# Optimization experiments

Measured on AMD Instinct MI355X. Metric: run time of the kernel, lower is better.

The kernel has to match this reference:

```python
import jax, jax.numpy as jnp
import numpy as np

WIDTH = 768
HEAD = 64

def setup_inputs() -> dict:
    key = jax.random.key(0)
    ks = jax.random.split(key, 8)
    x = jax.random.normal(ks[0], (8, 2048, WIDTH), dtype=jnp.float32)
    mask = jax.random.randint(ks[1], (2048, 2048), 0, 2, dtype=jnp.int32)
    s = 1.0 / np.sqrt(WIDTH)
    Wq = jax.random.normal(ks[2], (WIDTH, HEAD), dtype=jnp.float32) * s
    Wk = jax.random.normal(ks[3], (WIDTH, HEAD), dtype=jnp.float32) * s
    Wv = jax.random.normal(ks[4], (WIDTH, HEAD), dtype=jnp.float32) * s
    bq = jax.random.normal(ks[5], (HEAD,), dtype=jnp.float32) * 0.01
    bk = jax.random.normal(ks[6], (HEAD,), dtype=jnp.float32) * 0.01
    bv = jax.random.normal(ks[7], (HEAD,), dtype=jnp.float32) * 0.01
    return {"x": x, "Wq": Wq, "bq": bq, "Wk": Wk, "bk": bk, "Wv": Wv, "bv": bv, "mask": mask}

def reference(x, Wq, bq, Wk, bk, Wv, bv, mask) -> jnp.ndarray:
    # x: [B, N, width]; projections -> [B, N, head]
    Q = jnp.einsum('bnw,wh->bnh', x, Wq) + bq
    K = jnp.einsum('bnw,wh->bnh', x, Wk) + bk
    V = jnp.einsum('bnw,wh->bnh', x, Wv) + bv
    scale = 1.0 / jnp.sqrt(jnp.asarray(Q.shape[-1], dtype=Q.dtype))
    scores = jnp.einsum('bqh,bkh->bqk', Q, K) * scale  # [B, N, N]
    scores = jnp.where(mask == 0, -jnp.inf, scores)
    attn = jax.nn.softmax(scores, axis=-1)
    return jnp.einsum('bqk,bkh->bqh', attn, V)
```

## Files before the change

kernel.cpp:

```cpp
#include <hip/hip_runtime.h>

typedef short  s8v   __attribute__((ext_vector_type(8)));
typedef float  f32x4 __attribute__((ext_vector_type(4)));

#define SEQ 2048
#define WID 768

__device__ __forceinline__ unsigned fbits(float f) {
    union { float f; unsigned u; } v; v.f = f; return v.u;
}
__device__ __forceinline__ float bitsf(unsigned u) {
    union { unsigned u; float f; } v; v.u = u; return v.f;
}
__device__ __forceinline__ unsigned short f2b(float f) {
    unsigned u = fbits(f);
    return (unsigned short)((u + 0x7FFFu + ((u >> 16) & 1u)) >> 16);
}
__device__ __forceinline__ unsigned packRNE(float a, float b) {
    unsigned ta = fbits(a) + 0x7FFFu + ((fbits(a) >> 16) & 1u);
    unsigned tb = fbits(b) + 0x7FFFu + ((fbits(b) >> 16) & 1u);
    return __builtin_amdgcn_perm(tb, ta, 0x07060302u);
}
__device__ __forceinline__ unsigned packTRUNC(float a, float b) {
    return __builtin_amdgcn_perm(fbits(b), fbits(a), 0x07060302u);
}
__device__ __forceinline__ f32x4 zero4() { f32x4 z = {0.f, 0.f, 0.f, 0.f}; return z; }

__device__ __forceinline__ void async16(const unsigned short* g, unsigned short* l) {
    __builtin_amdgcn_global_load_lds(
        (const __attribute__((address_space(1))) unsigned int*)g,
        (__attribute__((address_space(3))) unsigned int*)l, 16, 0, 0);
}
__device__ __forceinline__ void async16f(const float* g, float* l) {
    __builtin_amdgcn_global_load_lds(
        (const __attribute__((address_space(1))) unsigned int*)g,
        (__attribute__((address_space(3))) unsigned int*)l, 16, 0, 0);
}

__global__ __launch_bounds__(256) void prep_kernel(
    const int* __restrict__ mask,
    const float* __restrict__ Wq, const float* __restrict__ Wk, const float* __restrict__ Wv,
    unsigned* __restrict__ PM, unsigned short* __restrict__ Wt)
{
    const int tid = threadIdx.x;
    const int blk = blockIdx.x;
    if (blk < 512) {
        const int gid  = blk * 4 + (tid >> 6);
        const int lane = tid & 63, quad = lane >> 4, c = lane & 15;
        const int qb = gid >> 5, kb = gid & 31;
        unsigned w = 0;
        #pragma unroll
        for (int mt = 0; mt < 2; ++mt)
            #pragma unroll
            for (int i = 0; i < 4; ++i) {
                const int q = qb * 32 + mt * 16 + quad * 4 + i;
                const int4 mm = *(const int4*)&mask[(size_t)q * SEQ + kb * 64 + 4 * c];
                if (mm.x) w |= 1u << (mt * 16 + i * 4 + 0);
                if (mm.y) w |= 1u << (mt * 16 + i * 4 + 1);
                if (mm.z) w |= 1u << (mt * 16 + i * 4 + 2);
                if (mm.w) w |= 1u << (mt * 16 + i * 4 + 3);
            }
        PM[(size_t)gid * 64 + lane] = w;
    } else {
        const int cid = (blk - 512) * 256 + tid;
        const int mat = cid / 12288;
        const int rem = cid - mat * 12288;
        const int k = rem >> 4, c4 = rem & 15;
        const float* Wm = (mat == 0) ? Wq : (mat == 1) ? Wk : Wv;
        float4 w = *(const float4*)&Wm[(size_t)k * 64 + c4 * 4];
        float wv4[4] = {w.x, w.y, w.z, w.w};
        #pragma unroll
        for (int j = 0; j < 4; ++j)
            Wt[(size_t)(mat * 64 + c4 * 4 + j) * WID + k] = f2b(wv4[j]);
    }
}

__global__ __launch_bounds__(256, 4) void qkv_proj_kernel(
    const float* __restrict__ x, const unsigned short* __restrict__ Wt,
    const float* __restrict__ bq, const float* __restrict__ bk, const float* __restrict__ bv,
    unsigned short* __restrict__ QF, unsigned short* __restrict__ KF,
    unsigned short* __restrict__ VF)
{
    __shared__ __align__(16) unsigned char SMEM[49152];
    float (*Xs)[WID]           = (float(*)[WID])SMEM;
    unsigned short (*Xb)[776]  = (unsigned short(*)[776])(SMEM + 8192);
    unsigned short (*St)[208]  = (unsigned short(*)[208])SMEM;

    const int tid = threadIdx.x;
    const int wv = tid >> 6, lane = tid & 63, quad = lane >> 4, c = lane & 15;
    const int rowb = blockIdx.x * 16;
    const int c0w  = wv * 48;

    const float* xsrc = x + (size_t)rowb * WID;
    #pragma unroll
    for (int t = 0; t < 12; ++t) {
        const int d = wv * 12 + t;
        async16f(xsrc + d * 256 + lane * 4, (float*)SMEM + d * 256);
    }

    float bias[3];
    #pragma unroll
    for (int nt = 0; nt < 3; ++nt) {
        int col = c0w + nt * 16 + c;
        const float* B = (col < 64) ? bq : (col < 128) ? bk : bv;
        bias[nt] = B[col & 63];
    }
    __syncthreads();

    {
        const int r = tid >> 4, cc0 = (tid & 15) * 48;
        float4 f[12];
        #pragma unroll
        for (int j = 0; j < 12; ++j) f[j] = *(float4*)&Xs[r][cc0 + 4 * j];
        __syncthreads();
        #pragma unroll
        for (int j = 0; j < 6; ++j) {
            uint4 w;
            w.x = packRNE(f[2*j].x,   f[2*j].y);
            w.y = packRNE(f[2*j].z,   f[2*j].w);
            w.z = packRNE(f[2*j+1].x, f[2*j+1].y);
            w.w = packRNE(f[2*j+1].z, f[2*j+1].w);
            *(uint4*)&Xb[r][cc0 + 8 * j] = w;
        }
    }
    __syncthreads();

    f32x4 acc[3];
    #pragma unroll
    for (int nt = 0; nt < 3; ++nt) acc[nt] = zero4();

    uint4 pw[2][3];
    #pragma unroll
    for (int u = 0; u < 2; ++u)
        #pragma unroll
        for (int nt = 0; nt < 3; ++nt)
            pw[u][nt] = *(const uint4*)&Wt[(size_t)(c0w + nt * 16 + c) * WID + u * 32 + quad * 8];

    #pragma unroll
    for (int kc = 0; kc < 24; ++kc) {
        s8v af = *(const s8v*)&Xb[c][kc * 32 + quad * 8];
        union { uint4 u; s8v v; } bf[3];
        #pragma unroll
        for (int nt = 0; nt < 3; ++nt) bf[nt].u = pw[kc & 1][nt];
        if (kc + 2 < 24) {
            #pragma unroll
            for (int nt = 0; nt < 3; ++nt)
                pw[kc & 1][nt] = *(const uint4*)&Wt[(size_t)(c0w + nt * 16 + c) * WID + (kc + 2) * 32 + quad * 8];
        }
        #pragma unroll
        for (int nt = 0; nt < 3; ++nt)
            acc[nt] = __builtin_amdgcn_mfma_f32_16x16x32_bf16(af, bf[nt].v, acc[nt], 0, 0, 0);
    }

    #pragma unroll
    for (int nt = 0; nt < 3; ++nt)
        #pragma unroll
        for (int i = 0; i < 4; ++i)
            St[quad * 4 + i][c0w + nt * 16 + c] = f2b(acc[nt][i] + bias[nt]);
    __syncthreads();

    const int kb  = rowb >> 6;
    const int q0k = (rowb & 63) >> 2;
    const int ks0 = (rowb & 63) >> 5;
    const int qd0 = (rowb & 31) >> 3;

    if (tid < 128) {
        const int ks = tid >> 6, l = tid & 63, qd = l >> 4, cc = l & 15;
        uint4 v = *(uint4*)&St[cc][ks * 32 + qd * 8];
        *(uint4*)&QF[(((size_t)(rowb >> 4)) * 2 + ks) * 512 + (size_t)l * 8] = v;
    } else {
        const int u = tid - 128;
        const int ks = u >> 6, nt = (u >> 4) & 3, qd = (u >> 2) & 3, cc = u & 3;
        uint4 v = *(uint4*)&St[4 * cc + nt][64 + ks * 32 + qd * 8];
        *(uint4*)&KF[(((size_t)kb * 8 + ks * 4 + nt) * 64 + qd * 16 + q0k + cc) * 8] = v;
    }
    if (tid < 128) {
        const int d = tid >> 1, jj = tid & 1, qd = qd0 + jj;
        const int nt = d >> 4, cc = d & 15;
        unsigned short p[8];
        #pragma unroll
        for (int s = 0; s < 8; ++s) p[s] = St[jj * 8 + s][128 + d];
        uint4 w;
        w.x = (unsigned)p[0] | ((unsigned)p[1] << 16);
        w.y = (unsigned)p[2] | ((unsigned)p[3] << 16);
        w.z = (unsigned)p[4] | ((unsigned)p[5] << 16);
        w.w = (unsigned)p[6] | ((unsigned)p[7] << 16);
        *(uint4*)&VF[(((size_t)kb * 8 + ks0 * 4 + nt) * 64 + qd * 16 + cc) * 8] = w;
    }
}

__global__ __launch_bounds__(1024, 4) void attn_kernel(
    const unsigned short* __restrict__ QF, const unsigned short* __restrict__ KF,
    const unsigned short* __restrict__ VF, const unsigned* __restrict__ PM,
    float* __restrict__ out)
{
    __shared__ unsigned short KVk[2][4][4096];
    __shared__ __align__(16) unsigned char PsOb[36864];
    __shared__ float Lbuf[64];
    unsigned short (*Ps)[16][72] = (unsigned short(*)[16][72])PsOb;
    float (*Obuf)[68]            = (float(*)[68])PsOb;

    const int tid = threadIdx.x;
    const int wv = tid >> 6, lane = tid & 63, quad = lane >> 4, c = lane & 15;
    const int sl = wv & 3, qg = wv >> 2, mt = qg & 1;
    const int blk = blockIdx.x;
    const int bb = blk & 7, qt = blk >> 3;
    const size_t qrow0 = (size_t)bb * SEQ + qt * 64;

    if (tid < 64) Lbuf[tid] = 0.f;

    s8v qf[2];
    {
        const size_t qgrp = (size_t)bb * 128 + qt * 4 + qg;
        #pragma unroll
        for (int ks = 0; ks < 2; ++ks)
            qf[ks] = *(const s8v*)&QF[(qgrp * 2 + ks) * 512 + (size_t)lane * 8];
    }

    f32x4 O[4];
    float lro[4];
    #pragma unroll
    for (int nt = 0; nt < 4; ++nt) O[nt] = zero4();
    #pragma unroll
    for (int i = 0; i < 4; ++i) lro[i] = 0.f;

    {
        const size_t kbg = (size_t)bb * 32 + sl * 8;
        #pragma unroll
        for (int r = 0; r < 2; ++r) {
            const int cn = qg * 2 + r;
            async16(KF + kbg * 4096 + cn * 512 + lane * 8, &KVk[0][sl][cn * 512]);
        }
    }
    unsigned pm = PM[(size_t)((qt * 2 + (qg >> 1)) * 32 + sl * 8) * 64 + lane];

    for (int kt = 0; kt < 8; ++kt) {
        __syncthreads();

        if (kt < 7) {
            const size_t kbg = (size_t)bb * 32 + sl * 8 + kt + 1;
            #pragma unroll
            for (int r = 0; r < 2; ++r) {
                const int cn = qg * 2 + r;
                async16(KF + kbg * 4096 + cn * 512 + lane * 8, &KVk[(kt + 1) & 1][sl][cn * 512]);
            }
        }
        const unsigned pmN = (kt < 7)
            ? PM[(size_t)((qt * 2 + (qg >> 1)) * 32 + sl * 8 + kt + 1) * 64 + lane] : 0u;

        f32x4 S[4];
        #pragma unroll
        for (int nt = 0; nt < 4; ++nt) S[nt] = zero4();
        #pragma unroll
        for (int ks = 0; ks < 2; ++ks) {
            s8v kfr[4];
            #pragma unroll
            for (int nt = 0; nt < 4; ++nt)
                kfr[nt] = *(const s8v*)&KVk[kt & 1][sl][((ks * 4 + nt) * 64 + lane) * 8];
            #pragma unroll
            for (int nt = 0; nt < 4; ++nt)
                S[nt] = __builtin_amdgcn_mfma_f32_16x16x32_bf16(qf[ks], kfr[nt], S[nt], 0, 0, 0);
        }

        const size_t kbg = (size_t)bb * 32 + sl * 8 + kt;
        s8v vf[8];
        #pragma unroll
        for (int ks = 0; ks < 2; ++ks)
            #pragma unroll
            for (int nt = 0; nt < 4; ++nt)
                vf[ks * 4 + nt] = *(const s8v*)&VF[(kbg * 8 + ks * 4 + nt) * 512 + (size_t)lane * 8];

        const unsigned pmh = pm >> (mt * 16);
        #pragma unroll
        for (int i = 0; i < 4; ++i) {
            float p4[4];
            #pragma unroll
            for (int nt = 0; nt < 4; ++nt) {
                float e = exp2f(fmaf(S[nt][i], 0.18033688011112042f, -21.640425613334451f));
                p4[nt] = ((pmh >> (i * 4 + nt)) & 1u) ? e : 0.f;
            }
            unsigned u0 = packTRUNC(p4[0], p4[1]);
            unsigned u1 = packTRUNC(p4[2], p4[3]);
            lro[i] += bitsf(u0 << 16) + bitsf(u0 & 0xFFFF0000u)
                    + bitsf(u1 << 16) + bitsf(u1 & 0xFFFF0000u);
            *(uint2*)&Ps[wv][quad * 4 + i][4 * c] = make_uint2(u0, u1);
        }
        pm = pmN;

        #pragma unroll
        for (int ks = 0; ks < 2; ++ks) {
            s8v a = *(const s8v*)&Ps[wv][c][ks * 32 + quad * 8];
            #pragma unroll
            for (int nt = 0; nt < 4; ++nt)
                O[nt] = __builtin_amdgcn_mfma_f32_16x16x32_bf16(a, vf[ks * 4 + nt], O[nt], 0, 0, 0);
        }
    }

    __syncthreads();
    #pragma unroll
    for (int j = 0; j < 5; ++j) {
        int idx = tid + 1024 * j;
        if (idx < 64 * 68) ((float*)Obuf)[idx] = 0.f;
    }
    __syncthreads();
    #pragma unroll
    for (int i = 0; i < 4; ++i) {
        float l = lro[i];
        l += __shfl_xor(l, 1);
        l += __shfl_xor(l, 2);
        l += __shfl_xor(l, 4);
        l += __shfl_xor(l, 8);
        if (c == 0) atomicAdd(&Lbuf[qg * 16 + quad * 4 + i], l);
        #pragma unroll
        for (int nt = 0; nt < 4; ++nt)
            atomicAdd(&Obuf[qg * 16 + quad * 4 + i][nt * 16 + c], O[nt][i]);
    }
    __syncthreads();
    {
        const int r = tid >> 4, d4 = (tid & 15) * 4;
        const float invL = 1.0f / Lbuf[r];
        float4 v = *(float4*)&Obuf[r][d4];
        float4 o = make_float4(v.x * invL, v.y * invL, v.z * invL, v.w * invL);
        *(float4*)&out[(qrow0 + r) * 64 + d4] = o;
    }
}

extern "C" void kernel_launch(void* const* d_in, const int* in_sizes, int n_in,
                              void* d_out, int out_size, void* d_ws, size_t ws_size,
                              hipStream_t stream)
{
    const float* x    = (const float*)d_in[0];
    const float* Wq   = (const float*)d_in[1];
    const float* bq   = (const float*)d_in[2];
    const float* Wk   = (const float*)d_in[3];
    const float* bk   = (const float*)d_in[4];
    const float* Wv   = (const float*)d_in[5];
    const float* bv   = (const float*)d_in[6];
    const int*   mask = (const int*)d_in[7];
    float* out = (float*)d_out;

    unsigned short* QF = (unsigned short*)d_ws;
    unsigned short* KF = QF + (size_t)16384 * 64;
    unsigned short* VF = KF + (size_t)16384 * 64;
    unsigned short* Wt = VF + (size_t)16384 * 64;
    unsigned*       PM = (unsigned*)(Wt + (size_t)192 * WID);

    prep_kernel<<<656, 256, 0, stream>>>(mask, Wq, Wk, Wv, PM, Wt);
    qkv_proj_kernel<<<1024, 256, 0, stream>>>(x, Wt, bq, bk, bv, QF, KF, VF);
    attn_kernel<<<256, 1024, 0, stream>>>(QF, KF, VF, PM, out);
}
```

Measured before the change: 188.1 us.

## Pre-convert x to bf16 fragments and tile QKV projection with double-buffered LDS

Adds a conversion pass that writes x and the weights into bf16 MFMA-fragment layouts. The projection kernel becomes a 64-row-tile GEMM that double-buffers async LDS loads, so each weight tile is reused across more rows. The attention kernel now stages both K and V tiles into LDS with one async DMA per step instead of loading V straight from global memory into registers, at the cost of dropping K double buffering. The conversion pass adds an extra full read and write of x through global memory.

```diff
diff --git a/kernel.cpp b/kernel.cpp
--- a/kernel.cpp
+++ b/kernel.cpp
@@ -31,21 +31,31 @@
         (const __attribute__((address_space(1))) unsigned int*)g,
         (__attribute__((address_space(3))) unsigned int*)l, 16, 0, 0);
 }
-__device__ __forceinline__ void async16f(const float* g, float* l) {
-    __builtin_amdgcn_global_load_lds(
-        (const __attribute__((address_space(1))) unsigned int*)g,
-        (__attribute__((address_space(3))) unsigned int*)l, 16, 0, 0);
-}
-
-__global__ __launch_bounds__(256) void prep_kernel(
-    const int* __restrict__ mask,
+
+__global__ __launch_bounds__(256) void convert_kernel(
+    const float* __restrict__ x, const int* __restrict__ mask,
     const float* __restrict__ Wq, const float* __restrict__ Wk, const float* __restrict__ Wv,
-    unsigned* __restrict__ PM, unsigned short* __restrict__ Wt)
+    unsigned short* __restrict__ XF, unsigned short* __restrict__ WF,
+    unsigned* __restrict__ PM)
 {
     const int tid = threadIdx.x;
     const int blk = blockIdx.x;
-    if (blk < 512) {
-        const int gid  = blk * 4 + (tid >> 6);
+    if (blk < 6144) {
+        const unsigned s = blk * 256 + tid;
+        const unsigned g = s / 1536;
+        const unsigned r = s - g * 1536;
+        const unsigned kc32 = r >> 6, l = r & 63;
+        const unsigned row = g * 16 + (l & 15);
+        const unsigned k0 = kc32 * 32 + (l >> 4) * 8;
+        float4 f0 = *(const float4*)&x[(size_t)row * WID + k0];
+        float4 f1 = *(const float4*)&x[(size_t)row * WID + k0 + 4];
+        uint4 w;
+        w.x = packRNE(f0.x, f0.y); w.y = packRNE(f0.z, f0.w);
+        w.z = packRNE(f1.x, f1.y); w.w = packRNE(f1.z, f1.w);
+        *(uint4*)&XF[(size_t)s * 8] = w;
+    } else if (blk < 6656) {
+        const int b2 = blk - 6144;
+        const int gid  = b2 * 4 + (tid >> 6);
         const int lane = tid & 63, quad = lane >> 4, c = lane & 15;
         const int qb = gid >> 5, kb = gid & 31;
         unsigned w = 0;
@@ -62,130 +72,132 @@
             }
         PM[(size_t)gid * 64 + lane] = w;
     } else {
-        const int cid = (blk - 512) * 256 + tid;
-        const int mat = cid / 12288;
-        const int rem = cid - mat * 12288;
-        const int k = rem >> 4, c4 = rem & 15;
+        const int s2 = (blk - 6656) * 256 + tid;
+        const int chunk = s2 >> 6, l = s2 & 63;
+        const int ntg = chunk / 24, r = chunk - ntg * 24;
+        const int kc = r >> 1, h = r & 1;
+        const int mat = ntg >> 2;
+        const int col = (ntg & 3) * 16 + (l & 15);
+        const int k0 = kc * 64 + h * 32 + (l >> 4) * 8;
         const float* Wm = (mat == 0) ? Wq : (mat == 1) ? Wk : Wv;
-        float4 w = *(const float4*)&Wm[(size_t)k * 64 + c4 * 4];
-        float wv4[4] = {w.x, w.y, w.z, w.w};
-        #pragma unroll
-        for (int j = 0; j < 4; ++j)
-            Wt[(size_t)(mat * 64 + c4 * 4 + j) * WID + k] = f2b(wv4[j]);
-    }
-}
-
-__global__ __launch_bounds__(256, 4) void qkv_proj_kernel(
-    const float* __restrict__ x, const unsigned short* __restrict__ Wt,
+        float p[8];
+        #pragma unroll
+        for (int j = 0; j < 8; ++j) p[j] = Wm[(size_t)(k0 + j) * 64 + col];
+        uint4 w;
+        w.x = packRNE(p[0], p[1]); w.y = packRNE(p[2], p[3]);
+        w.z = packRNE(p[4], p[5]); w.w = packRNE(p[6], p[7]);
+        *(uint4*)&WF[(size_t)s2 * 8] = w;
+    }
+}
+
+__global__ __launch_bounds__(512, 4) void qkv_proj_kernel(
+    const unsigned short* __restrict__ XF, const unsigned short* __restrict__ WF,
     const float* __restrict__ bq, const float* __restrict__ bk, const float* __restrict__ bv,
     unsigned short* __restrict__ QF, unsigned short* __restrict__ KF,
     unsigned short* __restrict__ VF)
 {
-    __shared__ __align__(16) unsigned char SMEM[49152];
-    float (*Xs)[WID]           = (float(*)[WID])SMEM;
-    unsigned short (*Xb)[776]  = (unsigned short(*)[776])(SMEM + 8192);
-    unsigned short (*St)[208]  = (unsigned short(*)[208])SMEM;
+    __shared__ unsigned short AB[2][16384];
+    unsigned short (*St)[200] = (unsigned short(*)[200])AB;
 
     const int tid = threadIdx.x;
     const int wv = tid >> 6, lane = tid & 63, quad = lane >> 4, c = lane & 15;
-    const int rowb = blockIdx.x * 16;
-    const int c0w  = wv * 48;
-
-    const float* xsrc = x + (size_t)rowb * WID;
-    #pragma unroll
-    for (int t = 0; t < 12; ++t) {
-        const int d = wv * 12 + t;
-        async16f(xsrc + d * 256 + lane * 4, (float*)SMEM + d * 256);
-    }
+    const int rg = wv >> 2, cg = wv & 3;
+    const int blk = blockIdx.x;
+    const int g0 = blk * 4;
 
     float bias[3];
     #pragma unroll
     for (int nt = 0; nt < 3; ++nt) {
-        int col = c0w + nt * 16 + c;
+        int col = cg * 48 + nt * 16 + c;
         const float* B = (col < 64) ? bq : (col < 128) ? bk : bv;
         bias[nt] = B[col & 63];
     }
+
+    auto issue = [&](int kc, int b) {
+        #pragma unroll
+        for (int r = 0; r < 4; ++r) {
+            const int d = wv * 4 + r;
+            if (d < 8) {
+                const int gl = d >> 1, h = d & 1;
+                async16(XF + ((size_t)(g0 + gl) * 24 + 2 * kc + h) * 512 + lane * 8,
+                        &AB[b][(gl * 2 + h) * 512]);
+            } else {
+                const int e = d - 8, ntg = e >> 1, h = e & 1;
+                async16(WF + (((size_t)ntg * 12 + kc) * 2 + h) * 512 + lane * 8,
+                        &AB[b][4096 + (ntg * 2 + h) * 512]);
+            }
+        }
+    };
+
+    f32x4 acc[2][3];
+    #pragma unroll
+    for (int mt = 0; mt < 2; ++mt)
+        #pragma unroll
+        for (int nt = 0; nt < 3; ++nt) acc[mt][nt] = zero4();
+
+    issue(0, 0);
+    for (int kc = 0; kc < 12; ++kc) {
+        const int b = kc & 1;
+        __syncthreads();
+        if (kc < 11) issue(kc + 1, b ^ 1);
+
+        s8v afr[2][2], bfr[3][2];
+        #pragma unroll
+        for (int mt = 0; mt < 2; ++mt)
+            #pragma unroll
+            for (int h = 0; h < 2; ++h)
+                afr[mt][h] = *(const s8v*)&AB[b][((rg * 2 + mt) * 2 + h) * 512 + lane * 8];
+        #pragma unroll
+        for (int nt = 0; nt < 3; ++nt)
+            #pragma unroll
+            for (int h = 0; h < 2; ++h)
+                bfr[nt][h] = *(const s8v*)&AB[b][4096 + ((cg * 3 + nt) * 2 + h) * 512 + lane * 8];
+        #pragma unroll
+        for (int h = 0; h < 2; ++h)
+            #pragma unroll
+            for (int mt = 0; mt < 2; ++mt)
+                #pragma unroll
+                for (int nt = 0; nt < 3; ++nt)
+                    acc[mt][nt] = __builtin_amdgcn_mfma_f32_16x16x32_bf16(
+                        afr[mt][h], bfr[nt][h], acc[mt][nt], 0, 0, 0);
+        __syncthreads();
+    }
+
+    #pragma unroll
+    for (int mt = 0; mt < 2; ++mt)
+        #pragma unroll
+        for (int nt = 0; nt < 3; ++nt)
+            #pragma unroll
+            for (int i = 0; i < 4; ++i)
+                St[rg * 32 + mt * 16 + quad * 4 + i][cg * 48 + nt * 16 + c]
+                    = f2b(acc[mt][nt][i] + bias[nt]);
     __syncthreads();
 
     {
-        const int r = tid >> 4, cc0 = (tid & 15) * 48;
-        float4 f[12];
-        #pragma unroll
-        for (int j = 0; j < 12; ++j) f[j] = *(float4*)&Xs[r][cc0 + 4 * j];
-        __syncthreads();
-        #pragma unroll
-        for (int j = 0; j < 6; ++j) {
-            uint4 w;
-            w.x = packRNE(f[2*j].x,   f[2*j].y);
-            w.y = packRNE(f[2*j].z,   f[2*j].w);
-            w.z = packRNE(f[2*j+1].x, f[2*j+1].y);
-            w.w = packRNE(f[2*j+1].z, f[2*j+1].w);
-            *(uint4*)&Xb[r][cc0 + 8 * j] = w;
-        }
-    }
-    __syncthreads();
-
-    f32x4 acc[3];
-    #pragma unroll
-    for (int nt = 0; nt < 3; ++nt) acc[nt] = zero4();
-
-    uint4 pw[2][3];
-    #pragma unroll
-    for (int u = 0; u < 2; ++u)
-        #pragma unroll
-        for (int nt = 0; nt < 3; ++nt)
-            pw[u][nt] = *(const uint4*)&Wt[(size_t)(c0w + nt * 16 + c) * WID + u * 32 + quad * 8];
-
-    #pragma unroll
-    for (int kc = 0; kc < 24; ++kc) {
-        s8v af = *(const s8v*)&Xb[c][kc * 32 + quad * 8];
-        union { uint4 u; s8v v; } bf[3];
-        #pragma unroll
-        for (int nt = 0; nt < 3; ++nt) bf[nt].u = pw[kc & 1][nt];
-        if (kc + 2 < 24) {
-            #pragma unroll
-            for (int nt = 0; nt < 3; ++nt)
-                pw[kc & 1][nt] = *(const uint4*)&Wt[(size_t)(c0w + nt * 16 + c) * WID + (kc + 2) * 32 + quad * 8];
-        }
-        #pragma unroll
-        for (int nt = 0; nt < 3; ++nt)
-            acc[nt] = __builtin_amdgcn_mfma_f32_16x16x32_bf16(af, bf[nt].v, acc[nt], 0, 0, 0);
-    }
-
-    #pragma unroll
-    for (int nt = 0; nt < 3; ++nt)
-        #pragma unroll
-        for (int i = 0; i < 4; ++i)
-            St[quad * 4 + i][c0w + nt * 16 + c] = f2b(acc[nt][i] + bias[nt]);
-    __syncthreads();
-
-    const int kb  = rowb >> 6;
-    const int q0k = (rowb & 63) >> 2;
-    const int ks0 = (rowb & 63) >> 5;
-    const int qd0 = (rowb & 31) >> 3;
-
-    if (tid < 128) {
-        const int ks = tid >> 6, l = tid & 63, qd = l >> 4, cc = l & 15;
-        uint4 v = *(uint4*)&St[cc][ks * 32 + qd * 8];
-        *(uint4*)&QF[(((size_t)(rowb >> 4)) * 2 + ks) * 512 + (size_t)l * 8] = v;
-    } else {
-        const int u = tid - 128;
-        const int ks = u >> 6, nt = (u >> 4) & 3, qd = (u >> 2) & 3, cc = u & 3;
-        uint4 v = *(uint4*)&St[4 * cc + nt][64 + ks * 32 + qd * 8];
-        *(uint4*)&KF[(((size_t)kb * 8 + ks * 4 + nt) * 64 + qd * 16 + q0k + cc) * 8] = v;
-    }
-    if (tid < 128) {
-        const int d = tid >> 1, jj = tid & 1, qd = qd0 + jj;
-        const int nt = d >> 4, cc = d & 15;
+        const int g = tid >> 7, ks = (tid >> 6) & 1, l = tid & 63;
+        uint4 v = *(uint4*)&St[g * 16 + (l & 15)][ks * 32 + (l >> 4) * 8];
+        *(uint4*)&QF[(((size_t)(g0 + g)) * 2 + ks) * 512 + (size_t)l * 8] = v;
+    }
+    {
+        const int ksnt = tid >> 6, l = tid & 63;
+        const int ks = ksnt >> 2, nt = ksnt & 3;
+        uint4 v = *(uint4*)&St[4 * (l & 15) + nt][64 + ks * 32 + (l >> 4) * 8];
+        *(uint4*)&KF[(((size_t)blk * 8 + ksnt) * 64 + l) * 8] = v;
+    }
+    {
+        const int ksnt = tid >> 6, l = tid & 63;
+        const int ks = ksnt >> 2, nt = ksnt & 3;
+        const int d = 128 + nt * 16 + (l & 15);
+        const int r0 = ks * 32 + (l >> 4) * 8;
         unsigned short p[8];
         #pragma unroll
-        for (int s = 0; s < 8; ++s) p[s] = St[jj * 8 + s][128 + d];
+        for (int s = 0; s < 8; ++s) p[s] = St[r0 + s][d];
         uint4 w;
         w.x = (unsigned)p[0] | ((unsigned)p[1] << 16);
         w.y = (unsigned)p[2] | ((unsigned)p[3] << 16);
         w.z = (unsigned)p[4] | ((unsigned)p[5] << 16);
         w.w = (unsigned)p[6] | ((unsigned)p[7] << 16);
-        *(uint4*)&VF[(((size_t)kb * 8 + ks0 * 4 + nt) * 64 + qd * 16 + cc) * 8] = w;
+        *(uint4*)&VF[(((size_t)blk * 8 + ksnt) * 64 + l) * 8] = w;
     }
 }
 
@@ -194,7 +206,7 @@
     const unsigned short* __restrict__ VF, const unsigned* __restrict__ PM,
     float* __restrict__ out)
 {
-    __shared__ unsigned short KVk[2][4][4096];
+    __shared__ unsigned short KV[4][8192];
     __shared__ __align__(16) unsigned char PsOb[36864];
     __shared__ float Lbuf[64];
     unsigned short (*Ps)[16][72] = (unsigned short(*)[16][72])PsOb;
@@ -224,29 +236,22 @@
     #pragma unroll
     for (int i = 0; i < 4; ++i) lro[i] = 0.f;
 
-    {
-        const size_t kbg = (size_t)bb * 32 + sl * 8;
-        #pragma unroll
-        for (int r = 0; r < 2; ++r) {
-            const int cn = qg * 2 + r;
-            async16(KF + kbg * 4096 + cn * 512 + lane * 8, &KVk[0][sl][cn * 512]);
-        }
-    }
-    unsigned pm = PM[(size_t)((qt * 2 + (qg >> 1)) * 32 + sl * 8) * 64 + lane];
-
+    auto kv_dma = [&](int kt) {
+        const size_t kbg = (size_t)bb * 32 + sl * 8 + kt;
+        #pragma unroll
+        for (int r = 0; r < 4; ++r) {
+            const int d = qg * 4 + r;
+            const unsigned short* src = (d < 8)
+                ? KF + kbg * 4096 + (d & 7) * 512 + lane * 8
+                : VF + kbg * 4096 + (d & 7) * 512 + lane * 8;
+            async16(src, &KV[sl][(d >> 3) * 4096 + (d & 7) * 512]);
+        }
+    };
+
+    kv_dma(0);
     for (int kt = 0; kt < 8; ++kt) {
+        const unsigned pm = PM[(size_t)((qt * 2 + (qg >> 1)) * 32 + sl * 8 + kt) * 64 + lane];
         __syncthreads();
-
-        if (kt < 7) {
-            const size_t kbg = (size_t)bb * 32 + sl * 8 + kt + 1;
-            #pragma unroll
-            for (int r = 0; r < 2; ++r) {
-                const int cn = qg * 2 + r;
-                async16(KF + kbg * 4096 + cn * 512 + lane * 8, &KVk[(kt + 1) & 1][sl][cn * 512]);
-            }
-        }
-        const unsigned pmN = (kt < 7)
-            ? PM[(size_t)((qt * 2 + (qg >> 1)) * 32 + sl * 8 + kt + 1) * 64 + lane] : 0u;
 
         f32x4 S[4];
         #pragma unroll
@@ -256,19 +261,11 @@
             s8v kfr[4];
             #pragma unroll
             for (int nt = 0; nt < 4; ++nt)
-                kfr[nt] = *(const s8v*)&KVk[kt & 1][sl][((ks * 4 + nt) * 64 + lane) * 8];
+                kfr[nt] = *(const s8v*)&KV[sl][((ks * 4 + nt) * 64 + lane) * 8];
             #pragma unroll
             for (int nt = 0; nt < 4; ++nt)
                 S[nt] = __builtin_amdgcn_mfma_f32_16x16x32_bf16(qf[ks], kfr[nt], S[nt], 0, 0, 0);
         }
-
-        const size_t kbg = (size_t)bb * 32 + sl * 8 + kt;
-        s8v vf[8];
-        #pragma unroll
-        for (int ks = 0; ks < 2; ++ks)
-            #pragma unroll
-            for (int nt = 0; nt < 4; ++nt)
-                vf[ks * 4 + nt] = *(const s8v*)&VF[(kbg * 8 + ks * 4 + nt) * 512 + (size_t)lane * 8];
 
         const unsigned pmh = pm >> (mt * 16);
         #pragma unroll
@@ -285,18 +282,22 @@
                     + bitsf(u1 << 16) + bitsf(u1 & 0xFFFF0000u);
             *(uint2*)&Ps[wv][quad * 4 + i][4 * c] = make_uint2(u0, u1);
         }
-        pm = pmN;
 
         #pragma unroll
         for (int ks = 0; ks < 2; ++ks) {
             s8v a = *(const s8v*)&Ps[wv][c][ks * 32 + quad * 8];
+            s8v vfr[4];
             #pragma unroll
             for (int nt = 0; nt < 4; ++nt)
-                O[nt] = __builtin_amdgcn_mfma_f32_16x16x32_bf16(a, vf[ks * 4 + nt], O[nt], 0, 0, 0);
-        }
-    }
-
-    __syncthreads();
+                vfr[nt] = *(const s8v*)&KV[sl][4096 + ((ks * 4 + nt) * 64 + lane) * 8];
+            #pragma unroll
+            for (int nt = 0; nt < 4; ++nt)
+                O[nt] = __builtin_amdgcn_mfma_f32_16x16x32_bf16(a, vfr[nt], O[nt], 0, 0, 0);
+        }
+        __syncthreads();
+        if (kt < 7) kv_dma(kt + 1);
+    }
+
     #pragma unroll
     for (int j = 0; j < 5; ++j) {
         int idx = tid + 1024 * j;
@@ -342,10 +343,11 @@
     unsigned short* QF = (unsigned short*)d_ws;
     unsigned short* KF = QF + (size_t)16384 * 64;
     unsigned short* VF = KF + (size_t)16384 * 64;
-    unsigned short* Wt = VF + (size_t)16384 * 64;
-    unsigned*       PM = (unsigned*)(Wt + (size_t)192 * WID);
-
-    prep_kernel<<<656, 256, 0, stream>>>(mask, Wq, Wk, Wv, PM, Wt);
-    qkv_proj_kernel<<<1024, 256, 0, stream>>>(x, Wt, bq, bk, bv, QF, KF, VF);
+    unsigned short* XF = VF + (size_t)16384 * 64;
+    unsigned short* WF = XF + (size_t)16384 * WID;
+    unsigned*       PM = (unsigned*)(WF + (size_t)192 * WID);
+
+    convert_kernel<<<6728, 256, 0, stream>>>(x, mask, Wq, Wk, Wv, XF, WF, PM);
+    qkv_proj_kernel<<<256, 512, 0, stream>>>(XF, WF, bq, bk, bv, QF, KF, VF);
     attn_kernel<<<256, 1024, 0, stream>>>(QF, KF, VF, PM, out);
 }
```

Measured after the change: 162.9 us. 1.15x faster.
